# Kernel optimization log

Measured on AMD Instinct MI355X. Metric: run time of the kernel, lower is better.

The kernel has to match this reference:

```python
import jax, jax.numpy as jnp
import numpy as np

N_NODES, N_EDGES = 5000, 50000
NUM_BASIS, CUTOFF, RADIAL_DIM = 8, 5.0, 64
NODE_EMBED, MAX_Z = 64, 100
NUM_NEIGHBORS = 10.0
PI = float(np.pi)

IRREPS_EDGE = [(1, 0, 1), (1, 1, -1), (1, 2, 1)]      # 1x0e + 1x1o + 1x2e (dim 9)
IRREPS_INIT = [(64, 0, 1)]                            # 64x0e
IRREPS_HID  = [(32, 0, 1), (16, 1, -1), (8, 2, 1)]    # 32x0e + 16x1o + 8x2e (dim 120)

def _offsets(irr):
    offs, o = [], 0
    for m, l, p in irr:
        offs.append(o); o += m * (2 * l + 1)
    return offs

def _sh_blocks(v, xp):
    # real spherical harmonics, component normalization, m = -l..l, v must be unit
    x, y, z = v[..., 0], v[..., 1], v[..., 2]
    s3, s5, s15 = 3.0 ** 0.5, 5.0 ** 0.5, 15.0 ** 0.5
    Y0 = xp.ones(v.shape[:-1] + (1,), dtype=v.dtype)
    Y1 = xp.stack([y, z, x], axis=-1) * s3
    Y2 = xp.stack([s15 * x * y, s15 * y * z, 0.5 * s5 * (3.0 * z * z - 1.0),
                   s15 * x * z, 0.5 * s15 * (x * x - y * y)], axis=-1)
    return [Y0, Y1, Y2]

def _rand_rot(rng):
    q, _ = np.linalg.qr(rng.normal(size=(3, 3)))
    if np.linalg.det(q) < 0:
        q[:, 0] = -q[:, 0]
    return q

def _wigner_D(l, R, pts):
    A = _sh_blocks(pts, np)[l]
    B = _sh_blocks(pts @ R.T, np)[l]
    return np.linalg.lstsq(A, B, rcond=None)[0].T  # Y(R r) = D @ Y(r)

def _cg(l1, l2, l3):
    # unit-norm real Clebsch-Gordan tensor from null space of rotation invariance
    rng = np.random.default_rng(1000 + 100 * l1 + 10 * l2 + l3)
    pts = rng.normal(size=(256, 3)); pts /= np.linalg.norm(pts, axis=1, keepdims=True)
    d1, d2, d3 = 2 * l1 + 1, 2 * l2 + 1, 2 * l3 + 1
    rows = []
    for _ in range(3):
        R = _rand_rot(rng)
        K = np.kron(np.kron(_wigner_D(l1, R, pts), _wigner_D(l2, R, pts)), _wigner_D(l3, R, pts))
        rows.append(K - np.eye(d1 * d2 * d3))
    _, _, Vt = np.linalg.svd(np.vstack(rows))
    C = Vt[-1].reshape(d1, d2, d3)
    i = np.argmax(np.abs(C))
    if C.flat[i] < 0:
        C = -C
    return (C / np.linalg.norm(C)).astype(np.float32)

def _make_paths(irreps_in, irreps_out):
    paths, off = [], 0
    fan = [0] * len(irreps_out)
    for i1, (m1, l1, p1) in enumerate(irreps_in):
        for i2, (m2, l2, p2) in enumerate(IRREPS_EDGE):
            for i3, (m3, l3, p3) in enumerate(irreps_out):
                if abs(l1 - l2) <= l3 <= l1 + l2 and p1 * p2 == p3:
                    paths.append((i1, i2, i3, off))
                    off += m1 * m2 * m3
                    fan[i3] += m1 * m2
    return paths, off, fan

PATHS0, NUMEL0, FAN0 = _make_paths(IRREPS_INIT, IRREPS_HID)   # NUMEL0 = 3584
PATHS1, NUMEL1, FAN1 = _make_paths(IRREPS_HID, IRREPS_HID)    # NUMEL1 = 3456

CG = {}
for _paths, _irr_in in ((PATHS0, IRREPS_INIT), (PATHS1, IRREPS_HID)):
    for _i1, _i2, _i3, _ in _paths:
        _key = (_irr_in[_i1][1], IRREPS_EDGE[_i2][1], IRREPS_HID[_i3][1])
        if _key not in CG:
            CG[_key] = jnp.asarray(_cg(*_key))

EDGE_OFF = _offsets(IRREPS_EDGE)

def _tensor_product(x, sh, w, irreps_in, irreps_out, paths, fan):
    E = x.shape[0]
    in_off = _offsets(irreps_in)
    outs = [jnp.zeros((E, m * (2 * l + 1)), x.dtype) for m, l, p in irreps_out]
    for i1, i2, i3, off in paths:
        m1, l1, _ = irreps_in[i1]
        _, l2, _ = IRREPS_EDGE[i2]
        m3, l3, _ = irreps_out[i3]
        x1 = x[:, in_off[i1]:in_off[i1] + m1 * (2 * l1 + 1)].reshape(E, m1, 2 * l1 + 1)
        y = sh[:, EDGE_OFF[i2]:EDGE_OFF[i2] + 2 * l2 + 1]
        wb = w[:, off:off + m1 * m3].reshape(E, m1, m3)
        alpha = (2 * l3 + 1) ** 0.5 / float(fan[i3]) ** 0.5
        msg = jnp.einsum('eui,ej,ijk,euv->evk', x1, y, CG[(l1, l2, l3)], wb) * alpha
        outs[i3] = outs[i3] + msg.reshape(E, -1)
    return jnp.concatenate(outs, axis=1)

def _self_connection(x, ws, irreps_in, irreps_out):
    N = x.shape[0]
    in_off = _offsets(irreps_in)
    outs, wi = [], 0
    for m3, l3, p3 in irreps_out:
        hit = [j for j, (m1, l1, p1) in enumerate(irreps_in) if (l1, p1) == (l3, p3)]
        if hit:
            j = hit[0]
            m1, l1, _ = irreps_in[j]
            xb = x[:, in_off[j]:in_off[j] + m1 * (2 * l1 + 1)].reshape(N, m1, 2 * l1 + 1)
            yb = jnp.einsum('nui,uv->nvi', xb, ws[wi]) / float(m1) ** 0.5
            outs.append(yb.reshape(N, -1)); wi += 1
        else:
            outs.append(jnp.zeros((N, m3 * (2 * l3 + 1)), x.dtype))
    return jnp.concatenate(outs, axis=1)

def _forward(positions, embed, rad_w1, rad_b1, rad_w2, rad_b2,
             wnn0_w1, wnn0_w2, wnn1_w1, wnn1_w2,
             sc0_0e, sc1_0e, sc1_1o, sc1_2e,
             edge_vec, edge_len, atomic_numbers, edge_index):
    node = embed[atomic_numbers]                                  # (N, 64)
    src, dst = edge_index[0], edge_index[1]
    u = edge_vec / (edge_len[:, None] + 1e-8)                     # unit edge vectors
    sh = jnp.concatenate(_sh_blocks(u, jnp), axis=-1)             # (E, 9)
    # radial basis encoding: Bessel basis * smooth cosine cutoff -> MLP
    freqs = jnp.arange(1, NUM_BASIS + 1, dtype=edge_len.dtype) * (PI / CUTOFF)
    r = edge_len[:, None]
    basis = jnp.sin(freqs * r) / jnp.maximum(r, 1e-8)
    xr = edge_len / CUTOFF
    cut = jnp.where(xr < 1.0, 0.5 * (1.0 + jnp.cos(PI * xr)), 0.0)
    rad = jax.nn.silu((basis * cut[:, None]) @ rad_w1 + rad_b1) @ rad_w2 + rad_b2
    inv_sqrt_n = 1.0 / NUM_NEIGHBORS ** 0.5
    layers = [(IRREPS_INIT, PATHS0, FAN0, wnn0_w1, wnn0_w2, [sc0_0e], True),
              (IRREPS_HID, PATHS1, FAN1, wnn1_w1, wnn1_w2, [sc1_0e, sc1_1o, sc1_2e], False)]
    for irr_in, paths, fan, w1, w2, scs, do_act in layers:
        w = jax.nn.silu(rad @ w1) @ w2                            # per-edge TP weights
        msg = _tensor_product(node[src], sh, w, irr_in, IRREPS_HID, paths, fan)
        agg = jax.ops.segment_sum(msg, dst, num_segments=N_NODES) * inv_sqrt_n
        node = agg + _self_connection(node, scs, irr_in, IRREPS_HID)
        if do_act:                                                # silu on L=0 scalars only
            node = jnp.concatenate([jax.nn.silu(node[:, :32]), node[:, 32:]], axis=1)
    return node                                                   # (N, 120)

def setup_inputs():
    key = jax.random.key(0)
    ks = jax.random.split(key, 20)
    edge_vec = jax.random.normal(ks[0], (N_EDGES, 3), jnp.float32) * 1.5
    edge_len = jnp.linalg.norm(edge_vec, axis=-1)
    return {
        'positions': jax.random.normal(ks[1], (N_NODES, 3), jnp.float32) * 5.0,
        'embed': jax.random.normal(ks[2], (MAX_Z, NODE_EMBED), jnp.float32),
        'rad_w1': jax.random.normal(ks[3], (NUM_BASIS, 64), jnp.float32) / NUM_BASIS ** 0.5,
        'rad_b1': jnp.zeros((64,), jnp.float32),
        'rad_w2': jax.random.normal(ks[4], (64, RADIAL_DIM), jnp.float32) / 8.0,
        'rad_b2': jnp.zeros((RADIAL_DIM,), jnp.float32),
        'wnn0_w1': jax.random.normal(ks[5], (RADIAL_DIM, 64), jnp.float32) / 8.0,
        'wnn0_w2': jax.random.normal(ks[6], (64, NUMEL0), jnp.float32) / 8.0,
        'wnn1_w1': jax.random.normal(ks[7], (RADIAL_DIM, 64), jnp.float32) / 8.0,
        'wnn1_w2': jax.random.normal(ks[8], (64, NUMEL1), jnp.float32) / 8.0,
        'sc0_0e': jax.random.normal(ks[9], (64, 32), jnp.float32),
        'sc1_0e': jax.random.normal(ks[10], (32, 32), jnp.float32),
        'sc1_1o': jax.random.normal(ks[11], (16, 16), jnp.float32),
        'sc1_2e': jax.random.normal(ks[12], (8, 8), jnp.float32),
        'edge_vec': edge_vec,
        'edge_len': edge_len,
        'atomic_numbers': jax.random.randint(ks[13], (N_NODES,), 0, MAX_Z, jnp.int32),
        'edge_index': jax.random.randint(ks[14], (2, N_EDGES), 0, N_NODES, jnp.int32),
    }

def reference(positions, embed, rad_w1, rad_b1, rad_w2, rad_b2,
              wnn0_w1, wnn0_w2, wnn1_w1, wnn1_w2,
              sc0_0e, sc1_0e, sc1_1o, sc1_2e,
              edge_vec, edge_len, atomic_numbers, edge_index):
    return _forward(positions, embed, rad_w1, rad_b1, rad_w2, rad_b2,
                    wnn0_w1, wnn0_w2, wnn1_w1, wnn1_w2,
                    sc0_0e, sc1_0e, sc1_1o, sc1_2e,
                    edge_vec, edge_len, atomic_numbers, edge_index)
```

## Files before the change

kernel.cpp:

```cpp
#include <hip/hip_runtime.h>
#include <hip/hip_bf16.h>
#include <math.h>

#define E_EDGES 50000
#define NN 5000

typedef __hip_bfloat16 bf16;
typedef __attribute__((ext_vector_type(8))) short short8;
typedef __attribute__((ext_vector_type(4))) float f32x4;

__device__ __forceinline__ float b2f(bf16 v) { return __bfloat162float(v); }
__device__ __forceinline__ float siluf(float x) { return x / (1.0f + __expf(-x)); }
__device__ __forceinline__ float us2f(unsigned short u) {
  union { unsigned int i; float f; } c; c.i = ((unsigned int)u) << 16; return c.f;
}

__global__ void __launch_bounds__(256) k_setup(
    const float* __restrict__ evec, const float* __restrict__ elen,
    float* __restrict__ shb, float* __restrict__ bc,
    const float* __restrict__ w2, const float* __restrict__ b2,
    const float* __restrict__ w01, const float* __restrict__ w11,
    bf16* __restrict__ Mbb,
    float* __restrict__ bias0, float* __restrict__ bias1,
    const float* __restrict__ emb, const int* __restrict__ an,
    float* __restrict__ node0, bf16* __restrict__ node0b,
    const float* __restrict__ w0, bf16* __restrict__ W0rtb,
    const float* __restrict__ w1w2, bf16* __restrict__ W2t,
    const int* __restrict__ ei, int* __restrict__ hist, int* __restrict__ hist2) {
  const int b = blockIdx.x, tid = threadIdx.x;
  if (b < 196) {
    int e = b*256 + tid;
    if (e >= E_EDGES) return;
    atomicAdd(&hist[ei[e]], 1);
    atomicAdd(&hist2[ei[E_EDGES + e]], 1);
    float x = evec[3*e+0], y = evec[3*e+1], z = evec[3*e+2];
    float r = elen[e];
    float inv = 1.0f / (r + 1e-8f);
    float ux = x*inv, uy = y*inv, uz = z*inv;
    const float s3 = 1.7320508075688772f, s5 = 2.2360679774997896f, s15 = 3.8729833462074170f;
    float* sh = shb + (size_t)e*12;
    sh[0] = 1.0f;
    sh[1] = s3*uy; sh[2] = s3*uz; sh[3] = s3*ux;
    sh[4] = s15*ux*uy; sh[5] = s15*uy*uz; sh[6] = 0.5f*s5*(3.0f*uz*uz - 1.0f);
    sh[7] = s15*ux*uz; sh[8] = 0.5f*s15*(ux*ux - uy*uy);
    sh[9] = 0.f; sh[10] = 0.f; sh[11] = 0.f;
    float rr = fmaxf(r, 1e-8f);
    const float pi = 3.14159265358979f;
    float xr = r * 0.2f;
    float cut = (xr < 1.0f) ? 0.5f*(1.0f + cosf(pi*xr)) : 0.0f;
    float fb = pi * 0.2f;
    for (int k = 1; k <= 8; ++k)
      bc[(size_t)e*8 + (k-1)] = sinf(fb*(float)k*r)/rr * cut;
  } else if (b < 212) {
    int i = (b-196)*256 + tid;
    int hh = i >> 6, c = i & 63;
    float a0 = 0.f, a1 = 0.f;
    for (int j = 0; j < 64; ++j) {
      float wv = w2[hh*64 + j];
      a0 += wv * w01[j*64 + c];
      a1 += wv * w11[j*64 + c];
    }
    Mbb[(size_t)c*64 + hh]        = __float2bfloat16(a0);
    Mbb[(size_t)(64 + c)*64 + hh] = __float2bfloat16(a1);
    if (hh == 0) {
      float s0 = 0.f, s1 = 0.f;
      for (int j = 0; j < 64; ++j) {
        s0 += b2[j] * w01[j*64 + c];
        s1 += b2[j] * w11[j*64 + c];
      }
      bias0[c] = s0;
      bias1[c] = s1;
    }
  } else if (b < 1462) {
    int i = (b-212)*256 + tid;
    int n = i >> 6, c = i & 63;
    float v = emb[an[n]*64 + c];
    node0[i] = v;
    node0b[i] = __float2bfloat16(v);
  } else if (b < 2358) {
    int idx = (b-1462)*256 + tid;
    int col = idx >> 6, u = idx & 63;
    int hh = col / 56, vp = col - hh*56;
    int boff, m3, v;
    if (vp < 32)      { boff = 0;    m3 = 32; v = vp; }
    else if (vp < 48) { boff = 2048; m3 = 16; v = vp - 32; }
    else              { boff = 3072; m3 = 8;  v = vp - 48; }
    W0rtb[idx] = __float2bfloat16(w0[hh*3584 + boff + u*m3 + v]);
  } else {
    int idx = (b-2358)*256 + tid;
    int nn = idx >> 6, k = idx & 63;
    int p, loc;
    if (nn < 1024)      { p=0;  loc=nn;      }
    else if (nn < 1536) { p=1;  loc=nn-1024; }
    else if (nn < 1792) { p=2;  loc=nn-1536; }
    else if (nn < 2048) { p=3;  loc=nn-1792; }
    else if (nn < 2560) { p=4;  loc=nn-2048; }
    else if (nn < 2688) { p=5;  loc=nn-2560; }
    else if (nn < 2944) { p=6;  loc=nn-2688; }
    else if (nn < 3008) { p=7;  loc=nn-2944; }
    else if (nn < 3136) { p=8;  loc=nn-3008; }
    else if (nn < 3392) { p=9;  loc=nn-3136; }
    else                { p=10; loc=nn-3392; }
    const int M1s[11] = {32,32,32,16,16,16,16,8,8,8,8};
    const int M3s[11] = {32,16,8,16,32,8,16,8,16,32,8};
    int m1 = M1s[p], m3 = M3s[p];
    int v = loc / m1, u = loc - v*m1;
    int src = (nn - loc) + u*m3 + v;
    W2t[idx] = __float2bfloat16(w1w2[(size_t)k*3456 + src]);
  }
}

__global__ void __launch_bounds__(256) k_mid(
    const float* __restrict__ bc,
    const float* __restrict__ w1, const float* __restrict__ b1,
    const bf16* __restrict__ Mbb,
    const float* __restrict__ bias0, const float* __restrict__ bias1,
    float* __restrict__ q0, bf16* __restrict__ q1b,
    const int* __restrict__ hist, int* __restrict__ start,
    const int* __restrict__ hist2, int* __restrict__ start2) {
  __shared__ float smem[1024];
  __shared__ __align__(16) short sHb[2048];
  const int tid = threadIdx.x;
  const int b = blockIdx.x;
  if (b < 1563) {
    float* sW1 = smem;
    float* sB  = smem + 512;
    float* sb0 = smem + 576;
    float* sb1 = smem + 640;
    float* sBC = smem + 704;
    const int j = tid >> 6, m = tid & 63;
    for (int i = tid; i < 512; i += 256) sW1[i] = w1[i];
    if (tid < 64) { sB[tid] = b1[tid]; sb0[tid] = bias0[tid]; sb1[tid] = bias1[tid]; }
    {
      int e = b*32 + (tid >> 3);
      int k = tid & 7;
      int eL = e < E_EDGES ? e : E_EDGES-1;
      sBC[tid] = bc[(size_t)eL*8 + k];
    }
    __syncthreads();
    #pragma unroll
    for (int g = 0; g < 8; ++g) {
      int el = g*4 + j;
      float t = sB[m];
      #pragma unroll
      for (int k = 0; k < 8; ++k) t += sBC[el*8+k]*sW1[k*64+m];
      bf16 hv = __float2bfloat16(siluf(t));
      sHb[el*64 + m] = *(short*)&hv;
    }
    __syncthreads();
    const int w = tid >> 6, lane = tid & 63;
    const int row16 = lane & 15, quad = lane >> 4;
    const int mtile = w & 1, cg = w >> 1;
    const short* ap = sHb + (mtile*16 + row16)*64 + quad*8;
    short8 a0 = *(const short8*)ap;
    short8 a1 = *(const short8*)(ap + 32);
    f32x4 acc[4] = {};
    #pragma unroll
    for (int ni = 0; ni < 4; ++ni) {
      const short* bp = (const short*)Mbb + (size_t)(cg*64 + ni*16 + row16)*64 + quad*8;
      short8 b0 = *(const short8*)bp;
      short8 b1v = *(const short8*)(bp + 32);
      acc[ni] = __builtin_amdgcn_mfma_f32_16x16x32_bf16(a0, b0, acc[ni], 0,0,0);
      acc[ni] = __builtin_amdgcn_mfma_f32_16x16x32_bf16(a1, b1v, acc[ni], 0,0,0);
    }
    const float* bias = cg ? sb1 : sb0;
    #pragma unroll
    for (int ni = 0; ni < 4; ++ni) {
      int c = ni*16 + row16;
      float bv = bias[c];
      #pragma unroll
      for (int r = 0; r < 4; ++r) {
        int e = b*32 + mtile*16 + quad*4 + r;
        if (e < E_EDGES) {
          float val = siluf(acc[ni][r] + bv);
          if (cg == 0) q0[(size_t)e*64 + c] = val;
          else         q1b[(size_t)e*64 + c] = __float2bfloat16(val);
        }
      }
    }
  } else {
    const int* h = (b == 1563) ? hist : hist2;
    int* st      = (b == 1563) ? start : start2;
    int* sp = (int*)smem;
    int base = tid*20;
    int localsum = 0;
    for (int i = 0; i < 20; ++i) { int jj = base+i; localsum += (jj < NN) ? h[jj] : 0; }
    sp[tid] = localsum;
    __syncthreads();
    if (tid == 0) {
      int acc = 0;
      for (int i = 0; i < 256; ++i) { int t = sp[i]; sp[i] = acc; acc += t; }
    }
    __syncthreads();
    int run = sp[tid];
    for (int i = 0; i < 20; ++i) {
      int jj = base+i;
      if (jj < NN) { st[jj] = run; run += h[jj]; }
    }
    if (tid == 255) st[NN] = run;
  }
}

__global__ void __launch_bounds__(256) k_pre0(
    const int* __restrict__ ei,
    const int* __restrict__ start, int* __restrict__ cursor, int* __restrict__ perm,
    const int* __restrict__ start2, int* __restrict__ cursor2, int* __restrict__ perm2,
    const bf16* __restrict__ A, const bf16* __restrict__ B, bf16* __restrict__ out) {
  __shared__ short lds[4][32*64];
  const int b = blockIdx.x, tid = threadIdx.x;
  if (b < 196) {
    int e = b*256 + tid;
    if (e >= E_EDGES) return;
    int src = ei[e];
    perm[start[src] + atomicAdd(&cursor[src], 1)] = e;
    int dst = ei[E_EDGES + e];
    perm2[start2[dst] + atomicAdd(&cursor2[dst], 1)] = e;
  } else {
    const int bb = b - 196;
    const int wid = tid >> 6, lane = tid & 63;
    const int nt = (bb % 14)*4 + wid;
    const int r0 = (bb / 14)*32;
    const int row16 = lane & 15, quad = lane >> 4;
    short8 a[2][2];
    #pragma unroll
    for (int mi = 0; mi < 2; ++mi) {
      int r = r0 + mi*16 + row16;
      int rg = (r < NN) ? r : 0;
      const short* ap = (const short*)A + (size_t)rg*64 + quad*8;
      a[mi][0] = *(const short8*)(ap);
      a[mi][1] = *(const short8*)(ap + 32);
    }
    if (nt < 56) {
      f32x4 acc[4][2] = {};
      #pragma unroll
      for (int ni = 0; ni < 4; ++ni) {
        int col = nt*64 + ni*16 + row16;
        const short* bp = (const short*)B + (size_t)col*64 + quad*8;
        short8 b0 = *(const short8*)(bp);
        short8 b1 = *(const short8*)(bp + 32);
        #pragma unroll
        for (int mi = 0; mi < 2; ++mi) {
          acc[ni][mi] = __builtin_amdgcn_mfma_f32_16x16x32_bf16(a[mi][0], b0, acc[ni][mi], 0,0,0);
          acc[ni][mi] = __builtin_amdgcn_mfma_f32_16x16x32_bf16(a[mi][1], b1, acc[ni][mi], 0,0,0);
        }
      }
      #pragma unroll
      for (int ni = 0; ni < 4; ++ni)
        #pragma unroll
        for (int mi = 0; mi < 2; ++mi)
          #pragma unroll
          for (int rr = 0; rr < 4; ++rr) {
            bf16 hv = __float2bfloat16(acc[ni][mi][rr]);
            lds[wid][(mi*16 + quad*4 + rr)*64 + ni*16 + row16] = *(short*)&hv;
          }
    }
    __syncthreads();
    if (nt < 56) {
      #pragma unroll
      for (int it = 0; it < 4; ++it) {
        int unit = it*64 + lane;
        int rrow = unit >> 3;
        int cu = (unit & 7) * 8;
        int r = r0 + rrow;
        if (r < NN)
          *(uint4*)((short*)out + (size_t)r*3584 + nt*64 + cu) =
              *(const uint4*)&lds[wid][rrow*64 + cu];
      }
    }
  }
}

__global__ void __launch_bounds__(256) k_bgemm(
    const bf16* __restrict__ A, const bf16* __restrict__ B,
    bf16* __restrict__ out, int stride, int ntiles, int e0, int nE) {
  __shared__ short lds[4][32*64];
  const int tid = threadIdx.x;
  const int wid = tid >> 6, lane = tid & 63;
  const int nt = blockIdx.x*4 + wid;
  const int r0 = blockIdx.y*32;
  const int row16 = lane & 15, quad = lane >> 4;

  short8 a[2][2];
  #pragma unroll
  for (int mi = 0; mi < 2; ++mi) {
    int r = r0 + mi*16 + row16;
    int rg = e0 + ((r < nE) ? r : 0);
    const short* ap = (const short*)A + (size_t)rg*64 + quad*8;
    a[mi][0] = *(const short8*)(ap);
    a[mi][1] = *(const short8*)(ap + 32);
  }
  if (nt < ntiles) {
    f32x4 acc[4][2] = {};
    #pragma unroll
    for (int ni = 0; ni < 4; ++ni) {
      int col = nt*64 + ni*16 + row16;
      const short* bp = (const short*)B + (size_t)col*64 + quad*8;
      short8 b0 = *(const short8*)(bp);
      short8 b1 = *(const short8*)(bp + 32);
      #pragma unroll
      for (int mi = 0; mi < 2; ++mi) {
        acc[ni][mi] = __builtin_amdgcn_mfma_f32_16x16x32_bf16(a[mi][0], b0, acc[ni][mi], 0,0,0);
        acc[ni][mi] = __builtin_amdgcn_mfma_f32_16x16x32_bf16(a[mi][1], b1, acc[ni][mi], 0,0,0);
      }
    }
    #pragma unroll
    for (int ni = 0; ni < 4; ++ni)
      #pragma unroll
      for (int mi = 0; mi < 2; ++mi)
        #pragma unroll
        for (int rr = 0; rr < 4; ++rr) {
          bf16 hv = __float2bfloat16(acc[ni][mi][rr]);
          lds[wid][(mi*16 + quad*4 + rr)*64 + ni*16 + row16] = *(short*)&hv;
        }
  }
  __syncthreads();
  if (nt < ntiles) {
    #pragma unroll
    for (int it = 0; it < 4; ++it) {
      int unit = it*64 + lane;
      int rrow = unit >> 3;
      int cu = (unit & 7) * 8;
      int r = r0 + rrow;
      if (r < nE)
        *(uint4*)((short*)out + (size_t)r*stride + nt*64 + cu) =
            *(const uint4*)&lds[wid][rrow*64 + cu];
    }
  }
}

__global__ void __launch_bounds__(256) k_msg0z(
    const float* __restrict__ q0, const bf16* __restrict__ G0,
    const int* __restrict__ start, const int* __restrict__ perm,
    float* __restrict__ zbuf) {
  __shared__ uint4 g4[448];
  __shared__ float sq[4][64];
  const int n = blockIdx.x;
  const int tid = threadIdx.x;
  const int wv = tid >> 6, lane = tid & 63;
  const uint4* gr = (const uint4*)(G0 + (size_t)n*3584);
  for (int i = tid; i < 448; i += 256) g4[i] = gr[i];
  const int s0 = start[n], s1 = start[n+1];
  __syncthreads();
  const short* gs = (const short*)g4;
  for (int base = s0; base < s1; base += 4) {
    int idx = base + wv;
    if (idx < s1) {
      int e = perm[idx];
      sq[wv][lane] = q0[(size_t)e*64 + lane];
      float z = 0.f;
      if (lane < 56) {
        #pragma unroll
        for (int h = 0; h < 64; ++h)
          z += sq[wv][h]*us2f((unsigned short)gs[h*56 + lane]);
        zbuf[(size_t)e*56 + lane] = z;
      }
    }
  }
}

__global__ void k_agg0(const float* __restrict__ zbuf, const float* __restrict__ shb,
                       const int* __restrict__ start2, const int* __restrict__ perm2,
                       const float* __restrict__ node0, const float* __restrict__ sc00,
                       float* __restrict__ node1) {
  __shared__ float n0[64];
  int n = blockIdx.x, tid = threadIdx.x;
  if (tid < 64) n0[tid] = node0[(size_t)n*64 + tid];
  __syncthreads();
  if (tid >= 120) return;
  int c = tid, zi, shi;
  if (c < 32)      { zi = c; shi = -1; }
  else if (c < 80) { int j = c-32, v = j/3, k = j - v*3; zi = 32 + v; shi = 1 + k; }
  else             { int j = c-80, v = j/5, k = j - v*5; zi = 48 + v; shi = 4 + k; }
  float acc = 0.f;
  const int s0 = start2[n], s1 = start2[n+1];
  for (int idx = s0; idx < s1; ++idx) {
    int e = perm2[idx];
    float z = zbuf[(size_t)e*56 + zi];
    acc += (shi < 0) ? z : z*shb[(size_t)e*12 + shi];
  }
  acc *= 0.125f * 0.3162277660168379f;
  if (c < 32) {
    float s = 0.f;
    for (int u = 0; u < 64; ++u) s += n0[u]*sc00[u*32 + c];
    acc += s * 0.125f;
    acc = siluf(acc);
  }
  node1[(size_t)n*120 + c] = acc;
}

__global__ void __launch_bounds__(256) k_tp4(
    const bf16* __restrict__ wch, const float* __restrict__ node1,
    const float* __restrict__ shb, const int* __restrict__ ei,
    int e0, int nE, float* __restrict__ msg1) {
  __shared__ float tl[4][592];
  __shared__ float xl[4][120];
  __shared__ float shl[4][12];
  const int tid = threadIdx.x;
  const int wv = tid >> 6, lane = tid & 63;
  int elr = blockIdx.x*4 + wv;
  const bool live = elr < nE;
  const int el = live ? elr : nE-1;
  const int eg = e0 + el;
  const int src = ei[eg];

  for (int i = lane; i < 120; i += 64) xl[wv][i] = node1[(size_t)src*120 + i];
  if (lane < 12) shl[wv][lane] = shb[(size_t)eg*12 + lane];
  __syncthreads();

  {
    const float* x  = xl[wv];
    const float* sh = shl[wv];
    const float A = 0.3162277660168379f, Bc = 0.1825741858350554f, B2 = 0.3651483716701107f;
    const int I_[11] = {0,2,0,1,1,2, 0,1,2, 0,2};
    const int J_[11] = {2,0,1,0,2,1, 0,1,2, 0,2};
    const int K_[11] = {0,0,1,1,3,3, 2,2,2, 4,4};
    const float V_[11] = {A,A,A,A,A,A, -Bc,B2,-Bc, -A,A};
    for (int idx = lane; idx < 592; idx += 64) {
      float t = 0.0f;
      if (idx < 32)       { t = x[idx] * 0.1336306209562122f; }
      else if (idx < 128) { int j = idx-32,  u=j/3, k=j-u*3; t = x[u]*sh[1+k] * 0.1178511301977579f; }
      else if (idx < 288) { int j = idx-128, u=j/5, k=j-u*5; t = x[u]*sh[4+k] * 0.125f; }
      else if (idx < 336) { int j = idx-288, u=j/3, k=j-u*3; t = x[32+u*3+k] * 0.1178511301977579f; }
      else if (idx < 352) { int u = idx-336;
        t = (x[32+u*3]*sh[1] + x[32+u*3+1]*sh[2] + x[32+u*3+2]*sh[3]) * 0.0771516749810460f; }
      else if (idx < 432) { int j = idx-352, u=j/5, k=j-u*5;
        float s = 0.f;
        #pragma unroll
        for (int q = 0; q < 11; ++q) if (K_[q] == k)
          s += V_[q]*x[32+u*3+I_[q]]*sh[1+J_[q]];
        t = s * 0.2795084971874737f; }
      else if (idx < 480) { int j = idx-432, u=j/3, k=j-u*3;
        float s = 0.f;
        #pragma unroll
        for (int q = 0; q < 11; ++q) if (J_[q] == k)
          s += V_[q]*x[32+u*3+I_[q]]*sh[4+K_[q]];
        t = s * 0.2041241452319315f; }
      else if (idx < 520) { int j = idx-480, u=j/5, k=j-u*5; t = x[80+u*5+k] * 0.125f; }
      else if (idx < 544) { int j = idx-520, u=j/3, k=j-u*3;
        float s = 0.f;
        #pragma unroll
        for (int q = 0; q < 11; ++q) if (J_[q] == k)
          s += V_[q]*x[80+u*5+K_[q]]*sh[1+I_[q]];
        t = s * 0.2041241452319315f; }
      else if (idx < 552) { int u = idx-544;
        float s = 0.f;
        #pragma unroll
        for (int q = 0; q < 5; ++q) s += x[80+u*5+q]*sh[4+q];
        t = s * 0.0597614304667197f; }
      else { int j = idx-552, u=j/5, k=j-u*5;
        const float P = 0.2390457218668787f, Q = 0.2070196678027063f, R = 0.1195228609334394f;
        const int I2_[25] = {0,0,2, 0,0,1,1,3,3, 1,1,2, 1,1,4, 2, 2,3,3, 2,4,4, 3,3,4};
        const int J2_[25] = {0,2,0, 1,3,0,3,0,1, 1,2,1, 1,4,1, 2, 3,2,3, 4,2,4, 3,4,3};
        const int K2_[25] = {2,0,0, 3,1,3,0,1,0, 2,1,1, 4,1,1, 2, 3,3,2, 4,4,2, 4,3,3};
        const float V2_[25] = {P,P,P, -Q,-Q,-Q,-Q,-Q,-Q, -R,-R,-R, Q,Q,Q, -P,
                               -R,-R,-R, P,P,P, -Q,-Q,-Q};
        float s = 0.f;
        #pragma unroll
        for (int q = 0; q < 25; ++q) if (K2_[q] == k)
          s += V2_[q]*x[80+u*5+I2_[q]]*sh[4+J2_[q]];
        t = s * 0.2795084971874737f; }
      tl[wv][idx] = t;
    }
  }
  __syncthreads();

  const short* wrow = (const short*)wch + (size_t)el*3456;
  const float* t = tl[wv];
  float r0 = 0.f, r1 = 0.f, r2 = 0.f;
  #define PATHC(OFF, M1C, NKC, TOFFC, REG)                                  \
    { int v = lane / (NKC), k = lane - v*(NKC);                             \
      const short* wp = wrow + (OFF) + v*(M1C);                             \
      _Pragma("unroll")                                                     \
      for (int ub = 0; ub < (M1C)/8; ++ub) {                                \
        short8 w8 = *(const short8*)(wp + ub*8);                            \
        _Pragma("unroll")                                                   \
        for (int r = 0; r < 8; ++r)                                         \
          REG += us2f((unsigned short)w8[r]) * t[(TOFFC)+(ub*8+r)*(NKC)+k]; \
      } }
  if (lane < 32) {
    PATHC(0,    32, 1, 0,   r0)
    PATHC(2048, 16, 1, 336, r0)
    PATHC(3136,  8, 1, 544, r0)
  }
  if (lane < 48) {
    PATHC(1024, 32, 3, 32,  r1)
    PATHC(1792, 16, 3, 288, r1)
    PATHC(2688, 16, 3, 432, r1)
    PATHC(3008,  8, 3, 520, r1)
  }
  if (lane < 40) {
    PATHC(1536, 32, 5, 128, r2)
    PATHC(2560, 16, 5, 352, r2)
    PATHC(2944,  8, 5, 480, r2)
    PATHC(3392,  8, 5, 552, r2)
  }
  #undef PATHC

  if (live) {
    const float s = 0.3162277660168379f;
    float* mp = msg1 + (size_t)eg*120;
    if (lane < 32) mp[lane] = r0*s;
    if (lane < 48) mp[32 + lane] = r1*s;
    if (lane < 40) mp[80 + lane] = r2*s;
  }
}

__global__ void k_out(const float* __restrict__ msg1,
                      const int* __restrict__ start2, const int* __restrict__ perm2,
                      const float* __restrict__ node1,
                      const float* __restrict__ sc0e, const float* __restrict__ sc1o,
                      const float* __restrict__ sc2e, float* __restrict__ out) {
  __shared__ float x[120];
  int n = blockIdx.x, tid = threadIdx.x;
  if (tid < 120) x[tid] = node1[(size_t)n*120 + tid];
  __syncthreads();
  if (tid >= 120) return;
  float v = 0.f;
  const int s0 = start2[n], s1 = start2[n+1];
  for (int idx = s0; idx < s1; ++idx)
    v += msg1[(size_t)perm2[idx]*120 + tid];
  if (tid < 32) {
    float s = 0.f;
    for (int u = 0; u < 32; ++u) s += x[u]*sc0e[u*32 + tid];
    v += s * 0.1767766952966369f;
  } else if (tid < 80) {
    int jj = tid - 32, vv = jj/3, k = jj - vv*3;
    float s = 0.f;
    for (int u = 0; u < 16; ++u) s += x[32 + u*3 + k]*sc1o[u*16 + vv];
    v += s * 0.25f;
  } else {
    int jj = tid - 80, vv = jj/5, k = jj - vv*5;
    float s = 0.f;
    for (int u = 0; u < 8; ++u) s += x[80 + u*5 + k]*sc2e[u*8 + vv];
    v += s * 0.3535533905932738f;
  }
  out[(size_t)n*120 + tid] = v;
}

extern "C" void kernel_launch(void* const* d_in, const int* in_sizes, int n_in,
                              void* d_out, int out_size, void* d_ws, size_t ws_size,
                              hipStream_t stream) {
  const float* embed   = (const float*)d_in[1];
  const float* rad_w1  = (const float*)d_in[2];
  const float* rad_b1  = (const float*)d_in[3];
  const float* rad_w2  = (const float*)d_in[4];
  const float* rad_b2  = (const float*)d_in[5];
  const float* wnn0_w1 = (const float*)d_in[6];
  const float* wnn0_w2 = (const float*)d_in[7];
  const float* wnn1_w1 = (const float*)d_in[8];
  const float* wnn1_w2 = (const float*)d_in[9];
  const float* sc0_0e  = (const float*)d_in[10];
  const float* sc1_0e  = (const float*)d_in[11];
  const float* sc1_1o  = (const float*)d_in[12];
  const float* sc1_2e  = (const float*)d_in[13];
  const float* edge_vec = (const float*)d_in[14];
  const float* edge_len = (const float*)d_in[15];
  const int*  anum    = (const int*)d_in[16];
  const int*  ei      = (const int*)d_in[17];

  float* ws = (float*)d_ws;
  float* shbuf = ws;
  float* bc    = ws + 600000;
  bf16*  q1b   = (bf16*)(ws + 1000000);
  float* node0 = ws + 2600000;
  bf16*  node0b= (bf16*)(ws + 2920000);
  bf16*  W0rtb = (bf16*)(ws + 3080000);
  bf16*  W2t   = (bf16*)(ws + 3194688);
  bf16*  Mbb   = (bf16*)(ws + 3305280);
  float* bias0 = ws + 3309376;
  float* bias1 = ws + 3309440;
  int*   hist   = (int*)(ws + 3309504);
  int*   cursor = (int*)(ws + 3314504);
  int*   hist2  = (int*)(ws + 3319504);
  int*   cursor2= (int*)(ws + 3324504);
  int*   start  = (int*)(ws + 3329504);
  int*   start2 = (int*)(ws + 3334512);
  int*   perm   = (int*)(ws + 3339520);
  int*   perm2  = (int*)(ws + 3389520);
  float* node1 = ws + 3439520;
  float* msg1  = ws + 4039520;
  float* q0    = ws + 10039520;
  float* zbuf  = ws + 13239520;
  bf16*  G0    = (bf16*)(ws + 16039520);
  bf16*  wbuf  = (bf16*)(ws + 10039520);

  long long CH;
  if      (ws_size >= (10039520ull + 43200000ull)*4) CH = 25000;
  else if (ws_size >= (10039520ull + 21600000ull)*4) CH = 12500;
  else                                               CH = 6250;

  hipMemsetAsync(hist, 0, 20000*sizeof(int), stream);

  k_setup<<<3222, 256, 0, stream>>>(edge_vec, edge_len, shbuf, bc,
                                    rad_w2, rad_b2, wnn0_w1, wnn1_w1, Mbb, bias0, bias1,
                                    embed, anum, node0, node0b,
                                    wnn0_w2, W0rtb, wnn1_w2, W2t, ei, hist, hist2);
  k_mid<<<1565, 256, 0, stream>>>(bc, rad_w1, rad_b1, Mbb, bias0, bias1,
                                  q0, q1b, hist, start, hist2, start2);
  k_pre0<<<196 + 14*157, 256, 0, stream>>>(ei, start, cursor, perm,
                                           start2, cursor2, perm2,
                                           node0b, W0rtb, G0);
  k_msg0z<<<NN, 256, 0, stream>>>(q0, G0, start, perm, zbuf);
  k_agg0<<<NN, 128, 0, stream>>>(zbuf, shbuf, start2, perm2, node0, sc0_0e, node1);

  for (long long e0 = 0; e0 < E_EDGES; e0 += CH) {
    k_bgemm<<<dim3(14, (unsigned)((CH+31)/32), 1), 256, 0, stream>>>(q1b, W2t, wbuf, 3456, 54, (int)e0, (int)CH);
    k_tp4<<<(unsigned)((CH+3)/4), 256, 0, stream>>>(wbuf, node1, shbuf, ei, (int)e0, (int)CH, msg1);
  }
  k_out<<<NN, 128, 0, stream>>>(msg1, start2, perm2, node1, sc1_0e, sc1_1o, sc1_2e, (float*)d_out);
}
```

Baseline: 464.9 us.

## Fuse per-edge weight GEMM with tensor-product contraction in one kernel

Replaces the chunked k_bgemm + k_tp4 pair with a single k_fuse kernel that computes the per-edge bf16 MFMA weights for 16 edges into shared memory (with an XOR swizzle) and contracts them immediately against the tensor-product features. This removes writing and re-reading the large per-edge weight buffer (3456 bf16 per edge) through global memory and the chunk loop launches. In exchange it uses heavy LDS per block (~50KB), which limits occupancy, and accumulates with shared-memory atomics whose contraction loops have irregular per-tile work. It also relies on E being a multiple of 16 since there is no bounds check.

```diff
diff --git a/kernel.cpp b/kernel.cpp
--- a/kernel.cpp
+++ b/kernel.cpp
@@ -270,64 +270,6 @@
   }
 }
 
-__global__ void __launch_bounds__(256) k_bgemm(
-    const bf16* __restrict__ A, const bf16* __restrict__ B,
-    bf16* __restrict__ out, int stride, int ntiles, int e0, int nE) {
-  __shared__ short lds[4][32*64];
-  const int tid = threadIdx.x;
-  const int wid = tid >> 6, lane = tid & 63;
-  const int nt = blockIdx.x*4 + wid;
-  const int r0 = blockIdx.y*32;
-  const int row16 = lane & 15, quad = lane >> 4;
-
-  short8 a[2][2];
-  #pragma unroll
-  for (int mi = 0; mi < 2; ++mi) {
-    int r = r0 + mi*16 + row16;
-    int rg = e0 + ((r < nE) ? r : 0);
-    const short* ap = (const short*)A + (size_t)rg*64 + quad*8;
-    a[mi][0] = *(const short8*)(ap);
-    a[mi][1] = *(const short8*)(ap + 32);
-  }
-  if (nt < ntiles) {
-    f32x4 acc[4][2] = {};
-    #pragma unroll
-    for (int ni = 0; ni < 4; ++ni) {
-      int col = nt*64 + ni*16 + row16;
-      const short* bp = (const short*)B + (size_t)col*64 + quad*8;
-      short8 b0 = *(const short8*)(bp);
-      short8 b1 = *(const short8*)(bp + 32);
-      #pragma unroll
-      for (int mi = 0; mi < 2; ++mi) {
-        acc[ni][mi] = __builtin_amdgcn_mfma_f32_16x16x32_bf16(a[mi][0], b0, acc[ni][mi], 0,0,0);
-        acc[ni][mi] = __builtin_amdgcn_mfma_f32_16x16x32_bf16(a[mi][1], b1, acc[ni][mi], 0,0,0);
-      }
-    }
-    #pragma unroll
-    for (int ni = 0; ni < 4; ++ni)
-      #pragma unroll
-      for (int mi = 0; mi < 2; ++mi)
-        #pragma unroll
-        for (int rr = 0; rr < 4; ++rr) {
-          bf16 hv = __float2bfloat16(acc[ni][mi][rr]);
-          lds[wid][(mi*16 + quad*4 + rr)*64 + ni*16 + row16] = *(short*)&hv;
-        }
-  }
-  __syncthreads();
-  if (nt < ntiles) {
-    #pragma unroll
-    for (int it = 0; it < 4; ++it) {
-      int unit = it*64 + lane;
-      int rrow = unit >> 3;
-      int cu = (unit & 7) * 8;
-      int r = r0 + rrow;
-      if (r < nE)
-        *(uint4*)((short*)out + (size_t)r*stride + nt*64 + cu) =
-            *(const uint4*)&lds[wid][rrow*64 + cu];
-    }
-  }
-}
-
 __global__ void __launch_bounds__(256) k_msg0z(
     const float* __restrict__ q0, const bf16* __restrict__ G0,
     const int* __restrict__ start, const int* __restrict__ perm,
@@ -388,121 +330,245 @@
   node1[(size_t)n*120 + c] = acc;
 }
 
-__global__ void __launch_bounds__(256) k_tp4(
-    const bf16* __restrict__ wch, const float* __restrict__ node1,
-    const float* __restrict__ shb, const int* __restrict__ ei,
-    int e0, int nE, float* __restrict__ msg1) {
-  __shared__ float tl[4][592];
-  __shared__ float xl[4][120];
-  __shared__ float shl[4][12];
+
+static __device__ const int TM1[54] = {
+  32,32,32,32,32,32,32,32,32,32,32,32,32,32,32,32,
+  32,32,32,32,32,32,32,32,
+  32,32,32,32,
+  16,16,16,16,
+  16,16,16,16,16,16,16,16,
+  16,16,
+  16,16,16,16,
+  8,
+  8,8,
+  8,8,8,8,
+  8};
+static __device__ const int TNK[54] = {
+  1,1,1,1,1,1,1,1,1,1,1,1,1,1,1,1,
+  3,3,3,3,3,3,3,3,
+  5,5,5,5,
+  3,3,3,3,
+  1,1,1,1,1,1,1,1,
+  5,5,
+  3,3,3,3,
+  5,
+  3,3,
+  1,1,1,1,
+  5};
+static __device__ const int TTOF[54] = {
+  0,0,0,0,0,0,0,0,0,0,0,0,0,0,0,0,
+  32,32,32,32,32,32,32,32,
+  128,128,128,128,
+  288,288,288,288,
+  336,336,336,336,336,336,336,336,
+  352,352,
+  432,432,432,432,
+  480,
+  520,520,
+  544,544,544,544,
+  552};
+static __device__ const int TOUT[54] = {
+  0,2,4,6,8,10,12,14,16,18,20,22,24,26,28,30,
+  32,38,44,50,56,62,68,74,
+  80,90,100,110,
+  32,44,56,68,
+  0,4,8,12,16,20,24,28,
+  80,100,
+  32,44,56,68,
+  80,
+  32,56,
+  0,8,16,24,
+  80};
+static __device__ const int TIT[54] = {
+  32,32,32,32,32,32,32,32,32,32,32,32,32,32,32,32,
+  96,96,96,96,96,96,96,96,
+  160,160,160,160,
+  192,192,192,192,
+  64,64,64,64,64,64,64,64,
+  320,320,
+  192,192,192,192,
+  640,
+  384,384,
+  128,128,128,128,
+  640};
+
+__global__ void __launch_bounds__(256) k_fuse(
+    const bf16* __restrict__ q1b, const bf16* __restrict__ W2t,
+    const float* __restrict__ node1, const float* __restrict__ shb,
+    const int* __restrict__ ei, float* __restrict__ msg1) {
+  __shared__ __align__(16) float tls[16*593];
+  __shared__ float msgl[16*120];
+  __shared__ float shl[16*12];
+  __shared__ __align__(16) float wls[4*1024];
+  float* xl = wls;
+
   const int tid = threadIdx.x;
   const int wv = tid >> 6, lane = tid & 63;
-  int elr = blockIdx.x*4 + wv;
-  const bool live = elr < nE;
-  const int el = live ? elr : nE-1;
-  const int eg = e0 + el;
-  const int src = ei[eg];
-
-  for (int i = lane; i < 120; i += 64) xl[wv][i] = node1[(size_t)src*120 + i];
-  if (lane < 12) shl[wv][lane] = shb[(size_t)eg*12 + lane];
+  const int e0 = blockIdx.x * 16;
+  const int row16 = lane & 15, quad = lane >> 4;
+
+  {
+    int e = tid >> 4, c0 = tid & 15;
+    int src = ei[e0 + e];
+    const float* xp = node1 + (size_t)src*120;
+    for (int c = c0; c < 120; c += 16) xl[e*120 + c] = xp[c];
+    if (c0 < 12) shl[e*12 + c0] = shb[(size_t)(e0+e)*12 + c0];
+  }
+  for (int i = tid; i < 1920; i += 256) msgl[i] = 0.f;
+
+  const short* ap = (const short*)q1b + (size_t)(e0 + row16)*64 + quad*8;
+  short8 a0 = *(const short8*)ap;
+  short8 a1 = *(const short8*)(ap + 32);
+
   __syncthreads();
 
   {
-    const float* x  = xl[wv];
-    const float* sh = shl[wv];
     const float A = 0.3162277660168379f, Bc = 0.1825741858350554f, B2 = 0.3651483716701107f;
     const int I_[11] = {0,2,0,1,1,2, 0,1,2, 0,2};
     const int J_[11] = {2,0,1,0,2,1, 0,1,2, 0,2};
     const int K_[11] = {0,0,1,1,3,3, 2,2,2, 4,4};
     const float V_[11] = {A,A,A,A,A,A, -Bc,B2,-Bc, -A,A};
-    for (int idx = lane; idx < 592; idx += 64) {
-      float t = 0.0f;
-      if (idx < 32)       { t = x[idx] * 0.1336306209562122f; }
-      else if (idx < 128) { int j = idx-32,  u=j/3, k=j-u*3; t = x[u]*sh[1+k] * 0.1178511301977579f; }
-      else if (idx < 288) { int j = idx-128, u=j/5, k=j-u*5; t = x[u]*sh[4+k] * 0.125f; }
-      else if (idx < 336) { int j = idx-288, u=j/3, k=j-u*3; t = x[32+u*3+k] * 0.1178511301977579f; }
-      else if (idx < 352) { int u = idx-336;
-        t = (x[32+u*3]*sh[1] + x[32+u*3+1]*sh[2] + x[32+u*3+2]*sh[3]) * 0.0771516749810460f; }
-      else if (idx < 432) { int j = idx-352, u=j/5, k=j-u*5;
-        float s = 0.f;
+    for (int el = 0; el < 4; ++el) {
+      const int e = wv*4 + el;
+      const float* x  = xl + e*120;
+      const float* sh = shl + e*12;
+      float* tp = tls + e*593;
+      for (int idx = lane; idx < 592; idx += 64) {
+        float t = 0.0f;
+        if (idx < 32)       { t = x[idx] * 0.1336306209562122f; }
+        else if (idx < 128) { int j = idx-32,  u=j/3, k=j-u*3; t = x[u]*sh[1+k] * 0.1178511301977579f; }
+        else if (idx < 288) { int j = idx-128, u=j/5, k=j-u*5; t = x[u]*sh[4+k] * 0.125f; }
+        else if (idx < 336) { int j = idx-288, u=j/3, k=j-u*3; t = x[32+u*3+k] * 0.1178511301977579f; }
+        else if (idx < 352) { int u = idx-336;
+          t = (x[32+u*3]*sh[1] + x[32+u*3+1]*sh[2] + x[32+u*3+2]*sh[3]) * 0.0771516749810460f; }
+        else if (idx < 432) { int j = idx-352, u=j/5, k=j-u*5;
+          float s = 0.f;
+          #pragma unroll
+          for (int q = 0; q < 11; ++q) if (K_[q] == k)
+            s += V_[q]*x[32+u*3+I_[q]]*sh[1+J_[q]];
+          t = s * 0.2795084971874737f; }
+        else if (idx < 480) { int j = idx-432, u=j/3, k=j-u*3;
+          float s = 0.f;
+          #pragma unroll
+          for (int q = 0; q < 11; ++q) if (J_[q] == k)
+            s += V_[q]*x[32+u*3+I_[q]]*sh[4+K_[q]];
+          t = s * 0.2041241452319315f; }
+        else if (idx < 520) { int j = idx-480, u=j/5, k=j-u*5; t = x[80+u*5+k] * 0.125f; }
+        else if (idx < 544) { int j = idx-520, u=j/3, k=j-u*3;
+          float s = 0.f;
+          #pragma unroll
+          for (int q = 0; q < 11; ++q) if (J_[q] == k)
+            s += V_[q]*x[80+u*5+K_[q]]*sh[1+I_[q]];
+          t = s * 0.2041241452319315f; }
+        else if (idx < 552) { int u = idx-544;
+          float s = 0.f;
+          #pragma unroll
+          for (int q = 0; q < 5; ++q) s += x[80+u*5+q]*sh[4+q];
+          t = s * 0.0597614304667197f; }
+        else { int j = idx-552, u=j/5, k=j-u*5;
+          const float P = 0.2390457218668787f, Q = 0.2070196678027063f, R = 0.1195228609334394f;
+          const int I2_[25] = {0,0,2, 0,0,1,1,3,3, 1,1,2, 1,1,4, 2, 2,3,3, 2,4,4, 3,3,4};
+          const int J2_[25] = {0,2,0, 1,3,0,3,0,1, 1,2,1, 1,4,1, 2, 3,2,3, 4,2,4, 3,4,3};
+          const int K2_[25] = {2,0,0, 3,1,3,0,1,0, 2,1,1, 4,1,1, 2, 3,3,2, 4,4,2, 4,3,3};
+          const float V2_[25] = {P,P,P, -Q,-Q,-Q,-Q,-Q,-Q, -R,-R,-R, Q,Q,Q, -P,
+                                 -R,-R,-R, P,P,P, -Q,-Q,-Q};
+          float s = 0.f;
+          #pragma unroll
+          for (int q = 0; q < 25; ++q) if (K2_[q] == k)
+            s += V2_[q]*x[80+u*5+I2_[q]]*sh[4+J2_[q]];
+          t = s * 0.2795084971874737f; }
+        tp[idx] = t;
+      }
+    }
+  }
+  __syncthreads();
+
+  float* wl = wls + wv*1024;
+
+  short8 bf0[4], bf1[4];
+  {
+    const int ntp = wv;
+    #pragma unroll
+    for (int ni = 0; ni < 4; ++ni) {
+      const short* bp = (const short*)W2t + (size_t)(ntp*64 + ni*16 + row16)*64 + quad*8;
+      bf0[ni] = *(const short8*)bp;
+      bf1[ni] = *(const short8*)(bp + 32);
+    }
+  }
+
+  #define CONTRACT(NKC)                                                      \
+    for (int it = lane; it < items; it += 64) {                              \
+      int e = it & 15, s = it >> 4;                                          \
+      int vl = s / (NKC), k = s - vl*(NKC);                                  \
+      const float* tb = tls + e*593 + toff + k;                              \
+      const float* wb = wl + e*64;                                           \
+      int sz = (e & 7) << 2;                                                 \
+      int cb = vl*m1;                                                        \
+      float a2 = 0.f;                                                        \
+      for (int uu = 0; uu < m1; uu += 4) {                                   \
+        f32x4 w4 = *(const f32x4*)&wb[(cb + uu) ^ sz];                       \
+        a2 += w4[0]*tb[(uu+0)*(NKC)] + w4[1]*tb[(uu+1)*(NKC)]                \
+            + w4[2]*tb[(uu+2)*(NKC)] + w4[3]*tb[(uu+3)*(NKC)];               \
+      }                                                                      \
+      atomicAdd(&msgl[e*120 + tout + s], a2);                                \
+    }
+
+  for (int nt = wv; nt < 54; nt += 4) {
+    f32x4 acc[4] = {};
+    #pragma unroll
+    for (int ni = 0; ni < 4; ++ni) {
+      acc[ni] = __builtin_amdgcn_mfma_f32_16x16x32_bf16(a0, bf0[ni], acc[ni], 0,0,0);
+      acc[ni] = __builtin_amdgcn_mfma_f32_16x16x32_bf16(a1, bf1[ni], acc[ni], 0,0,0);
+    }
+    #pragma unroll
+    for (int ni = 0; ni < 4; ++ni)
+      #pragma unroll
+      for (int r = 0; r < 4; ++r) {
+        int e = quad*4 + r;
+        int c = ni*16 + row16;
+        wl[e*64 + (c ^ ((e & 7) << 2))] = acc[ni][r];
+      }
+    if (nt + 4 < 54) {
+      #pragma unroll
+      for (int ni = 0; ni < 4; ++ni) {
+        const short* bp = (const short*)W2t + (size_t)((nt+4)*64 + ni*16 + row16)*64 + quad*8;
+        bf0[ni] = *(const short8*)bp;
+        bf1[ni] = *(const short8*)(bp + 32);
+      }
+    }
+    const int m1 = TM1[nt], nk = TNK[nt], toff = TTOF[nt], tout = TOUT[nt], items = TIT[nt];
+    if (nk == 1) {
+      if (m1 == 32) {
+        int it = lane & 31, uh = lane >> 5;
+        int e = it & 15, vl = it >> 4;
+        const float* tb = tls + e*593 + toff;
+        const float* wb = wl + e*64;
+        int sz = (e & 7) << 2;
+        int cb = vl*32;
+        float a2 = 0.f;
         #pragma unroll
-        for (int q = 0; q < 11; ++q) if (K_[q] == k)
-          s += V_[q]*x[32+u*3+I_[q]]*sh[1+J_[q]];
-        t = s * 0.2795084971874737f; }
-      else if (idx < 480) { int j = idx-432, u=j/3, k=j-u*3;
-        float s = 0.f;
-        #pragma unroll
-        for (int q = 0; q < 11; ++q) if (J_[q] == k)
-          s += V_[q]*x[32+u*3+I_[q]]*sh[4+K_[q]];
-        t = s * 0.2041241452319315f; }
-      else if (idx < 520) { int j = idx-480, u=j/5, k=j-u*5; t = x[80+u*5+k] * 0.125f; }
-      else if (idx < 544) { int j = idx-520, u=j/3, k=j-u*3;
-        float s = 0.f;
-        #pragma unroll
-        for (int q = 0; q < 11; ++q) if (J_[q] == k)
-          s += V_[q]*x[80+u*5+K_[q]]*sh[1+I_[q]];
-        t = s * 0.2041241452319315f; }
-      else if (idx < 552) { int u = idx-544;
-        float s = 0.f;
-        #pragma unroll
-        for (int q = 0; q < 5; ++q) s += x[80+u*5+q]*sh[4+q];
-        t = s * 0.0597614304667197f; }
-      else { int j = idx-552, u=j/5, k=j-u*5;
-        const float P = 0.2390457218668787f, Q = 0.2070196678027063f, R = 0.1195228609334394f;
-        const int I2_[25] = {0,0,2, 0,0,1,1,3,3, 1,1,2, 1,1,4, 2, 2,3,3, 2,4,4, 3,3,4};
-        const int J2_[25] = {0,2,0, 1,3,0,3,0,1, 1,2,1, 1,4,1, 2, 3,2,3, 4,2,4, 3,4,3};
-        const int K2_[25] = {2,0,0, 3,1,3,0,1,0, 2,1,1, 4,1,1, 2, 3,3,2, 4,4,2, 4,3,3};
-        const float V2_[25] = {P,P,P, -Q,-Q,-Q,-Q,-Q,-Q, -R,-R,-R, Q,Q,Q, -P,
-                               -R,-R,-R, P,P,P, -Q,-Q,-Q};
-        float s = 0.f;
-        #pragma unroll
-        for (int q = 0; q < 25; ++q) if (K2_[q] == k)
-          s += V2_[q]*x[80+u*5+I2_[q]]*sh[4+J2_[q]];
-        t = s * 0.2795084971874737f; }
-      tl[wv][idx] = t;
-    }
-  }
+        for (int uu0 = 0; uu0 < 16; uu0 += 4) {
+          int uu = uh*16 + uu0;
+          f32x4 w4 = *(const f32x4*)&wb[(cb + uu) ^ sz];
+          a2 += w4[0]*tb[uu+0] + w4[1]*tb[uu+1] + w4[2]*tb[uu+2] + w4[3]*tb[uu+3];
+        }
+        a2 += __shfl_xor(a2, 32);
+        if (lane < 32) atomicAdd(&msgl[e*120 + tout + vl], a2);
+      } else {
+        CONTRACT(1)
+      }
+    } else if (nk == 3) {
+      CONTRACT(3)
+    } else {
+      CONTRACT(5)
+    }
+  }
+  #undef CONTRACT
+
   __syncthreads();
-
-  const short* wrow = (const short*)wch + (size_t)el*3456;
-  const float* t = tl[wv];
-  float r0 = 0.f, r1 = 0.f, r2 = 0.f;
-  #define PATHC(OFF, M1C, NKC, TOFFC, REG)                                  \
-    { int v = lane / (NKC), k = lane - v*(NKC);                             \
-      const short* wp = wrow + (OFF) + v*(M1C);                             \
-      _Pragma("unroll")                                                     \
-      for (int ub = 0; ub < (M1C)/8; ++ub) {                                \
-        short8 w8 = *(const short8*)(wp + ub*8);                            \
-        _Pragma("unroll")                                                   \
-        for (int r = 0; r < 8; ++r)                                         \
-          REG += us2f((unsigned short)w8[r]) * t[(TOFFC)+(ub*8+r)*(NKC)+k]; \
-      } }
-  if (lane < 32) {
-    PATHC(0,    32, 1, 0,   r0)
-    PATHC(2048, 16, 1, 336, r0)
-    PATHC(3136,  8, 1, 544, r0)
-  }
-  if (lane < 48) {
-    PATHC(1024, 32, 3, 32,  r1)
-    PATHC(1792, 16, 3, 288, r1)
-    PATHC(2688, 16, 3, 432, r1)
-    PATHC(3008,  8, 3, 520, r1)
-  }
-  if (lane < 40) {
-    PATHC(1536, 32, 5, 128, r2)
-    PATHC(2560, 16, 5, 352, r2)
-    PATHC(2944,  8, 5, 480, r2)
-    PATHC(3392,  8, 5, 552, r2)
-  }
-  #undef PATHC
-
-  if (live) {
-    const float s = 0.3162277660168379f;
-    float* mp = msg1 + (size_t)eg*120;
-    if (lane < 32) mp[lane] = r0*s;
-    if (lane < 48) mp[32 + lane] = r1*s;
-    if (lane < 40) mp[80 + lane] = r2*s;
-  }
+  const float s = 0.3162277660168379f;
+  for (int i = tid; i < 1920; i += 256)
+    msg1[(size_t)e0*120 + i] = msgl[i] * s;
 }
 
 __global__ void k_out(const float* __restrict__ msg1,
@@ -582,12 +648,6 @@
   float* q0    = ws + 10039520;
   float* zbuf  = ws + 13239520;
   bf16*  G0    = (bf16*)(ws + 16039520);
-  bf16*  wbuf  = (bf16*)(ws + 10039520);
-
-  long long CH;
-  if      (ws_size >= (10039520ull + 43200000ull)*4) CH = 25000;
-  else if (ws_size >= (10039520ull + 21600000ull)*4) CH = 12500;
-  else                                               CH = 6250;
 
   hipMemsetAsync(hist, 0, 20000*sizeof(int), stream);
 
@@ -603,9 +663,7 @@
   k_msg0z<<<NN, 256, 0, stream>>>(q0, G0, start, perm, zbuf);
   k_agg0<<<NN, 128, 0, stream>>>(zbuf, shbuf, start2, perm2, node0, sc0_0e, node1);
 
-  for (long long e0 = 0; e0 < E_EDGES; e0 += CH) {
-    k_bgemm<<<dim3(14, (unsigned)((CH+31)/32), 1), 256, 0, stream>>>(q1b, W2t, wbuf, 3456, 54, (int)e0, (int)CH);
-    k_tp4<<<(unsigned)((CH+3)/4), 256, 0, stream>>>(wbuf, node1, shbuf, ei, (int)e0, (int)CH, msg1);
-  }
+  k_fuse<<<3125, 256, 0, stream>>>(q1b, W2t, node1, shbuf, ei, msg1);
+
   k_out<<<NN, 128, 0, stream>>>(msg1, start2, perm2, node1, sc1_0e, sc1_1o, sc1_2e, (float*)d_out);
 }
```

Result: slower. 628.1 us (+35.1%).
